# Kernel optimization log

Hardware: AMD Instinct MI355X
Metric: run time of the kernel (lower is better)

## Reference

```python
import jax, jax.numpy as jnp
import numpy as np

N_NODES = 10000
N_EDGES = 320000
D_IN = 256
D_OUT = 256


def setup_inputs() -> dict:
    key = jax.random.key(0)
    k1, k2, k3, k4, k5, k6 = jax.random.split(key, 6)
    feat = jax.random.normal(k1, (N_NODES, D_IN), dtype=jnp.float32)
    eweight = jax.random.uniform(k2, (N_EDGES, 1), dtype=jnp.float32)
    # Linear(in_dim*2 -> out_dim): weight [out, 2*in], bias [out]
    W = jax.random.normal(k3, (D_OUT, 2 * D_IN), dtype=jnp.float32) / np.sqrt(2 * D_IN)
    b = jax.random.normal(k4, (D_OUT,), dtype=jnp.float32) * 0.01
    src = jax.random.randint(k5, (N_EDGES,), 0, N_NODES, dtype=jnp.int64)
    dst = jax.random.randint(k6, (N_EDGES,), 0, N_NODES, dtype=jnp.int64)
    return {"feat": feat, "eweight": eweight, "W": W, "b": b, "src": src, "dst": dst}


def reference(feat, eweight, W, b, src, dst):
    n = feat.shape[0]
    # message: u_mul_e -> h[src] * ew   (broadcast [E,1] over [E,D])
    msg = feat[src] * eweight
    # mean reduce by destination: sum(msg) / in-degree
    agg = jax.ops.segment_sum(msg, dst, num_segments=n)
    deg = jax.ops.segment_sum(jnp.ones((src.shape[0],), dtype=feat.dtype), dst, num_segments=n)
    h_neigh = agg / jnp.maximum(deg, 1.0)[:, None]
    # concat aggregated with self features, then linear
    h = jnp.concatenate([h_neigh, feat], axis=-1)  # [N, 2*D]
    return h @ W.T + b
```

## Files before the change

### kernel.cpp

```cpp
#include <hip/hip_runtime.h>
#include <hip/hip_bf16.h>

#define N_NODES 10000
#define N_EDGES 320000
#define D 256
#define K_TOT 512
#define CAP 128

typedef __attribute__((ext_vector_type(8))) short bf16x8;
typedef __attribute__((ext_vector_type(4))) float f32x4;

__device__ __forceinline__ float bf2f(unsigned short u) {
  return __uint_as_float(((unsigned int)u) << 16);
}
__device__ __forceinline__ unsigned short f2bf(float f) {
  unsigned int x = __float_as_uint(f);
  unsigned int r = (x + 0x7fffu + ((x >> 16) & 1u)) >> 16;
  return (unsigned short)r;
}

#define FEAT_VECS (N_NODES * D / 8)
#define W_VECS    (D * K_TOT / 8)
#define CUR_VECS  (N_NODES / 4)
__global__ __launch_bounds__(256) void tobf16_kernel(
    const float* __restrict__ feat, const float* __restrict__ W,
    unsigned short* __restrict__ hcat, unsigned short* __restrict__ Wb,
    int* __restrict__ cursor) {
  int gid = blockIdx.x * 256 + threadIdx.x;
  const float* srcp;
  unsigned short* dstp;
  if (gid < FEAT_VECS) {
    int row = gid >> 5;
    int v = gid & 31;
    srcp = feat + (size_t)row * D + v * 8;
    dstp = hcat + (size_t)row * K_TOT + D + v * 8;
  } else if (gid < FEAT_VECS + W_VECS) {
    int g = gid - FEAT_VECS;
    int row = g >> 6;
    int v = g & 63;
    srcp = W + (size_t)row * K_TOT + v * 8;
    dstp = Wb + (size_t)row * K_TOT + v * 8;
  } else if (gid < FEAT_VECS + W_VECS + CUR_VECS) {
    int g = gid - (FEAT_VECS + W_VECS);
    reinterpret_cast<int4*>(cursor)[g] = make_int4(0, 0, 0, 0);
    return;
  } else {
    return;
  }
  float4 a = reinterpret_cast<const float4*>(srcp)[0];
  float4 b = reinterpret_cast<const float4*>(srcp)[1];
  reinterpret_cast<ushort4*>(dstp)[0] =
      make_ushort4(f2bf(a.x), f2bf(a.y), f2bf(a.z), f2bf(a.w));
  reinterpret_cast<ushort4*>(dstp)[1] =
      make_ushort4(f2bf(b.x), f2bf(b.y), f2bf(b.z), f2bf(b.w));
}

__global__ __launch_bounds__(256) void append_kernel(const int* __restrict__ src,
                                                     const int* __restrict__ dst,
                                                     const float* __restrict__ ew,
                                                     int* __restrict__ cursor,
                                                     int2* __restrict__ bucket) {
  int i = (blockIdx.x * 256 + threadIdx.x) * 2;
  if (i + 1 < N_EDGES) {
    int2 s2 = *reinterpret_cast<const int2*>(src + i);
    int2 d2 = *reinterpret_cast<const int2*>(dst + i);
    float2 w2 = *reinterpret_cast<const float2*>(ew + i);
    int pos0 = atomicAdd(&cursor[d2.x], 1);
    if (pos0 < CAP)
      bucket[(size_t)d2.x * CAP + pos0] = make_int2(s2.x, __float_as_int(w2.x));
    int pos1 = atomicAdd(&cursor[d2.y], 1);
    if (pos1 < CAP)
      bucket[(size_t)d2.y * CAP + pos1] = make_int2(s2.y, __float_as_int(w2.y));
  } else if (i < N_EDGES) {
    int d = dst[i];
    int pos = atomicAdd(&cursor[d], 1);
    if (pos < CAP)
      bucket[(size_t)d * CAP + pos] = make_int2(src[i], __float_as_int(ew[i]));
  }
}

__global__ __launch_bounds__(256) void agg_kernel(const int* __restrict__ cursor,
                                                  const int2* __restrict__ bucket,
                                                  unsigned short* __restrict__ hcat) {
  int bid = blockIdx.x;
  int half = (bid >= 2500) ? 1 : 0;
  int nb = bid - half * 2500;
  int wave = threadIdx.x >> 6;
  int lane = threadIdx.x & 63;
  int node = nb * 4 + wave;
  if (node >= N_NODES) return;
  int cnt = cursor[node];
  int end = min(cnt, CAP);
  const int2* bk = bucket + (size_t)node * CAP;
  const unsigned short* fb = hcat + D + half * 128 + (size_t)lane * 2;
  float a0 = 0.f, a1 = 0.f;
  int i = 0;

#define G2(p, va, vb)                                                          \
    va = *reinterpret_cast<const ushort2*>(fb + (size_t)(p).x * K_TOT);        \
    vb = *reinterpret_cast<const ushort2*>(fb + (size_t)(p).z * K_TOT);
#define A1(v, wgt)                                                             \
    a0 += bf2f((v).x) * (wgt); a1 += bf2f((v).y) * (wgt);
#define AP(p, va, vb)                                                          \
    { float wa_ = __int_as_float((p).y), wb_ = __int_as_float((p).w);          \
      A1(va, wa_) A1(vb, wb_) }

  for (; i + 16 <= end; i += 16) {
    int4 p0 = *reinterpret_cast<const int4*>(bk + i);
    int4 p1 = *reinterpret_cast<const int4*>(bk + i + 2);
    int4 p2 = *reinterpret_cast<const int4*>(bk + i + 4);
    int4 p3 = *reinterpret_cast<const int4*>(bk + i + 6);
    int4 p4 = *reinterpret_cast<const int4*>(bk + i + 8);
    int4 p5 = *reinterpret_cast<const int4*>(bk + i + 10);
    int4 p6 = *reinterpret_cast<const int4*>(bk + i + 12);
    int4 p7 = *reinterpret_cast<const int4*>(bk + i + 14);
    ushort2 v0, v1, v2, v3, v4, v5, v6, v7, v8, v9, va, vb, vc, vd, ve, vf;
    G2(p0, v0, v1) G2(p1, v2, v3) G2(p2, v4, v5) G2(p3, v6, v7)
    G2(p4, v8, v9) G2(p5, va, vb) G2(p6, vc, vd) G2(p7, ve, vf)
    AP(p0, v0, v1) AP(p1, v2, v3) AP(p2, v4, v5) AP(p3, v6, v7)
    AP(p4, v8, v9) AP(p5, va, vb) AP(p6, vc, vd) AP(p7, ve, vf)
  }
  for (; i + 8 <= end; i += 8) {
    int4 p0 = *reinterpret_cast<const int4*>(bk + i);
    int4 p1 = *reinterpret_cast<const int4*>(bk + i + 2);
    int4 p2 = *reinterpret_cast<const int4*>(bk + i + 4);
    int4 p3 = *reinterpret_cast<const int4*>(bk + i + 6);
    ushort2 v0, v1, v2, v3, v4, v5, v6, v7;
    G2(p0, v0, v1) G2(p1, v2, v3) G2(p2, v4, v5) G2(p3, v6, v7)
    AP(p0, v0, v1) AP(p1, v2, v3) AP(p2, v4, v5) AP(p3, v6, v7)
  }
  for (; i < end; ++i) {
    int2 sw = bk[i];
    ushort2 v = *reinterpret_cast<const ushort2*>(fb + (size_t)sw.x * K_TOT);
    float wgt = __int_as_float(sw.y);
    A1(v, wgt)
  }
#undef G2
#undef A1
#undef AP

  float inv = 1.0f / fmaxf((float)cnt, 1.0f);
  ushort2 o;
  o.x = f2bf(a0 * inv);
  o.y = f2bf(a1 * inv);
  *reinterpret_cast<ushort2*>(hcat + (size_t)node * K_TOT + half * 128 + lane * 2) = o;
}

#define GBM 64
#define GBN 64
#define GBK 64
#define LPAD 72
#define RTILES 157

__global__ __launch_bounds__(256) void gemm_kernel(
    const unsigned short* __restrict__ hcat, const unsigned short* __restrict__ Wb,
    const float* __restrict__ bias, float* __restrict__ out) {
  __shared__ unsigned short As[GBM][LPAD];
  __shared__ unsigned short Bs[GBN][LPAD];

  int bid = blockIdx.x;
  int r, c;
  if (bid < 608) {
    int g = bid >> 5;
    int w8 = bid & 31;
    r = g * 8 + (w8 & 7);
    c = w8 >> 3;
  } else {
    int w8 = bid - 608;
    r = 152 + w8 % 5;
    c = w8 / 5;
  }
  int row0 = r * GBM;
  int col0 = c * GBN;

  int t = threadIdx.x;
  int lane = t & 63;
  int w = t >> 6;
  int wr = w >> 1;
  int wc = w & 1;
  int lhi = lane >> 4;
  int llo = lane & 15;

  f32x4 acc[2][2];
  #pragma unroll
  for (int m = 0; m < 2; ++m)
    #pragma unroll
    for (int n = 0; n < 2; ++n) acc[m][n] = (f32x4){0.f, 0.f, 0.f, 0.f};

  for (int k0 = 0; k0 < K_TOT; k0 += GBK) {
    #pragma unroll
    for (int it = 0; it < 2; ++it) {
      int idx = t + it * 256;
      int rr = idx >> 3;
      int kv = (idx & 7) * 8;
      int row = row0 + rr;
      uint4 v = make_uint4(0, 0, 0, 0);
      if (row < N_NODES)
        v = *reinterpret_cast<const uint4*>(hcat + (size_t)row * K_TOT + k0 + kv);
      *reinterpret_cast<uint4*>(&As[rr][kv]) = v;
    }
    #pragma unroll
    for (int it = 0; it < 2; ++it) {
      int idx = t + it * 256;
      int cc = idx >> 3;
      int kv = (idx & 7) * 8;
      uint4 v = *reinterpret_cast<const uint4*>(Wb + (size_t)(col0 + cc) * K_TOT + k0 + kv);
      *reinterpret_cast<uint4*>(&Bs[cc][kv]) = v;
    }
    __syncthreads();

    #pragma unroll
    for (int ks = 0; ks < 2; ++ks) {
      int ak = ks * 32 + lhi * 8;
      bf16x8 a[2], b[2];
      #pragma unroll
      for (int m = 0; m < 2; ++m)
        a[m] = *reinterpret_cast<const bf16x8*>(&As[wr * 32 + m * 16 + llo][ak]);
      #pragma unroll
      for (int n = 0; n < 2; ++n)
        b[n] = *reinterpret_cast<const bf16x8*>(&Bs[wc * 32 + n * 16 + llo][ak]);
      #pragma unroll
      for (int m = 0; m < 2; ++m)
        #pragma unroll
        for (int n = 0; n < 2; ++n)
          acc[m][n] = __builtin_amdgcn_mfma_f32_16x16x32_bf16(a[m], b[n], acc[m][n], 0, 0, 0);
    }
    __syncthreads();
  }

  #pragma unroll
  for (int m = 0; m < 2; ++m) {
    #pragma unroll
    for (int n = 0; n < 2; ++n) {
      int col = col0 + wc * 32 + n * 16 + llo;
      float bv = bias[col];
      #pragma unroll
      for (int rr = 0; rr < 4; ++rr) {
        int orow = row0 + wr * 32 + m * 16 + lhi * 4 + rr;
        if (orow < N_NODES)
          out[(size_t)orow * D + col] = acc[m][n][rr] + bv;
      }
    }
  }
}

extern "C" void kernel_launch(void* const* d_in, const int* in_sizes, int n_in,
                              void* d_out, int out_size, void* d_ws, size_t ws_size,
                              hipStream_t stream) {
  const float* feat = (const float*)d_in[0];
  const float* ew   = (const float*)d_in[1];
  const float* W    = (const float*)d_in[2];
  const float* bias = (const float*)d_in[3];
  const int*   src  = (const int*)d_in[4];
  const int*   dst  = (const int*)d_in[5];
  float* out = (float*)d_out;

  char* ws = (char*)d_ws;
  unsigned short* hcat = (unsigned short*)ws;  ws += (size_t)N_NODES * K_TOT * sizeof(unsigned short);
  unsigned short* Wb   = (unsigned short*)ws;  ws += (size_t)D * K_TOT * sizeof(unsigned short);
  int* cursor   = (int*)ws;                    ws += N_NODES * sizeof(int);
  int2* bucket  = (int2*)ws;                   ws += (size_t)N_NODES * CAP * sizeof(int2);

  tobf16_kernel<<<(FEAT_VECS + W_VECS + CUR_VECS + 255) / 256, 256, 0, stream>>>(
      feat, W, hcat, Wb, cursor);
  append_kernel<<<(N_EDGES / 2 + 255) / 256, 256, 0, stream>>>(src, dst, ew, cursor, bucket);
  agg_kernel<<<5000, 256, 0, stream>>>(cursor, bucket, hcat);

  gemm_kernel<<<RTILES * 4, 256, 0, stream>>>(hcat, Wb, bias, out);
}
```

Baseline: 70.87 us.

## Slice bf16 features into column-sliced layout for cache-local gather aggregation

The conversion kernel now also writes a copy of bf16 features in a slice-major layout (8 slices of 32 columns), so each slice forms a compact table that is more likely to fit in cache. The aggregation kernel is split into 8 column slices per node group; in each wave, four groups of 16 lanes handle different edges in parallel and combine their partial sums with shuffles. This is meant to improve L2 locality of the random gathers and raise edge-level parallelism, at the cost of an extra feature copy write, more blocks, and re-reading the bucket lists once per slice.

Result: slower. 84.54 us (+19.3%).

```diff
diff --git a/kernel.cpp b/kernel.cpp
--- a/kernel.cpp
+++ b/kernel.cpp
@@ -6,6 +6,8 @@
 #define D 256
 #define K_TOT 512
 #define CAP 128
+#define NSLICE 8
+#define SCH 32
 
 typedef __attribute__((ext_vector_type(8))) short bf16x8;
 typedef __attribute__((ext_vector_type(4))) float f32x4;
@@ -24,35 +26,38 @@
 #define CUR_VECS  (N_NODES / 4)
 __global__ __launch_bounds__(256) void tobf16_kernel(
     const float* __restrict__ feat, const float* __restrict__ W,
-    unsigned short* __restrict__ hcat, unsigned short* __restrict__ Wb,
-    int* __restrict__ cursor) {
+    unsigned short* __restrict__ featb, unsigned short* __restrict__ hcat,
+    unsigned short* __restrict__ Wb, int* __restrict__ cursor) {
   int gid = blockIdx.x * 256 + threadIdx.x;
-  const float* srcp;
-  unsigned short* dstp;
   if (gid < FEAT_VECS) {
     int row = gid >> 5;
     int v = gid & 31;
-    srcp = feat + (size_t)row * D + v * 8;
-    dstp = hcat + (size_t)row * K_TOT + D + v * 8;
+    const float* srcp = feat + (size_t)row * D + v * 8;
+    float4 a = reinterpret_cast<const float4*>(srcp)[0];
+    float4 b = reinterpret_cast<const float4*>(srcp)[1];
+    ushort4 o0 = make_ushort4(f2bf(a.x), f2bf(a.y), f2bf(a.z), f2bf(a.w));
+    ushort4 o1 = make_ushort4(f2bf(b.x), f2bf(b.y), f2bf(b.z), f2bf(b.w));
+    unsigned short* dh = hcat + (size_t)row * K_TOT + D + v * 8;
+    reinterpret_cast<ushort4*>(dh)[0] = o0;
+    reinterpret_cast<ushort4*>(dh)[1] = o1;
+    int s = v >> 2;
+    unsigned short* ds = featb + ((size_t)s * N_NODES + row) * SCH + (v & 3) * 8;
+    reinterpret_cast<ushort4*>(ds)[0] = o0;
+    reinterpret_cast<ushort4*>(ds)[1] = o1;
   } else if (gid < FEAT_VECS + W_VECS) {
     int g = gid - FEAT_VECS;
-    int row = g >> 6;
-    int v = g & 63;
-    srcp = W + (size_t)row * K_TOT + v * 8;
-    dstp = Wb + (size_t)row * K_TOT + v * 8;
+    const float* srcp = W + (size_t)g * 8;
+    unsigned short* dstp = Wb + (size_t)g * 8;
+    float4 a = reinterpret_cast<const float4*>(srcp)[0];
+    float4 b = reinterpret_cast<const float4*>(srcp)[1];
+    reinterpret_cast<ushort4*>(dstp)[0] =
+        make_ushort4(f2bf(a.x), f2bf(a.y), f2bf(a.z), f2bf(a.w));
+    reinterpret_cast<ushort4*>(dstp)[1] =
+        make_ushort4(f2bf(b.x), f2bf(b.y), f2bf(b.z), f2bf(b.w));
   } else if (gid < FEAT_VECS + W_VECS + CUR_VECS) {
     int g = gid - (FEAT_VECS + W_VECS);
     reinterpret_cast<int4*>(cursor)[g] = make_int4(0, 0, 0, 0);
-    return;
-  } else {
-    return;
-  }
-  float4 a = reinterpret_cast<const float4*>(srcp)[0];
-  float4 b = reinterpret_cast<const float4*>(srcp)[1];
-  reinterpret_cast<ushort4*>(dstp)[0] =
-      make_ushort4(f2bf(a.x), f2bf(a.y), f2bf(a.z), f2bf(a.w));
-  reinterpret_cast<ushort4*>(dstp)[1] =
-      make_ushort4(f2bf(b.x), f2bf(b.y), f2bf(b.z), f2bf(b.w));
+  }
 }
 
 __global__ __launch_bounds__(256) void append_kernel(const int* __restrict__ src,
@@ -81,69 +86,53 @@
 
 __global__ __launch_bounds__(256) void agg_kernel(const int* __restrict__ cursor,
                                                   const int2* __restrict__ bucket,
+                                                  const unsigned short* __restrict__ featb,
                                                   unsigned short* __restrict__ hcat) {
-  int bid = blockIdx.x;
-  int half = (bid >= 2500) ? 1 : 0;
-  int nb = bid - half * 2500;
-  int wave = threadIdx.x >> 6;
+  int b = blockIdx.x;
+  int s = b & 7;
+  int g = b >> 3;
+  int wv = threadIdx.x >> 6;
   int lane = threadIdx.x & 63;
-  int node = nb * 4 + wave;
-  if (node >= N_NODES) return;
+  int node = g * 4 + wv;
+  int q = lane >> 4;
+  int c2 = lane & 15;
   int cnt = cursor[node];
   int end = min(cnt, CAP);
   const int2* bk = bucket + (size_t)node * CAP;
-  const unsigned short* fb = hcat + D + half * 128 + (size_t)lane * 2;
+  const unsigned short* fs = featb + (size_t)s * N_NODES * SCH + c2 * 2;
   float a0 = 0.f, a1 = 0.f;
-  int i = 0;
-
-#define G2(p, va, vb)                                                          \
-    va = *reinterpret_cast<const ushort2*>(fb + (size_t)(p).x * K_TOT);        \
-    vb = *reinterpret_cast<const ushort2*>(fb + (size_t)(p).z * K_TOT);
-#define A1(v, wgt)                                                             \
-    a0 += bf2f((v).x) * (wgt); a1 += bf2f((v).y) * (wgt);
-#define AP(p, va, vb)                                                          \
-    { float wa_ = __int_as_float((p).y), wb_ = __int_as_float((p).w);          \
-      A1(va, wa_) A1(vb, wb_) }
-
-  for (; i + 16 <= end; i += 16) {
-    int4 p0 = *reinterpret_cast<const int4*>(bk + i);
-    int4 p1 = *reinterpret_cast<const int4*>(bk + i + 2);
-    int4 p2 = *reinterpret_cast<const int4*>(bk + i + 4);
-    int4 p3 = *reinterpret_cast<const int4*>(bk + i + 6);
-    int4 p4 = *reinterpret_cast<const int4*>(bk + i + 8);
-    int4 p5 = *reinterpret_cast<const int4*>(bk + i + 10);
-    int4 p6 = *reinterpret_cast<const int4*>(bk + i + 12);
-    int4 p7 = *reinterpret_cast<const int4*>(bk + i + 14);
-    ushort2 v0, v1, v2, v3, v4, v5, v6, v7, v8, v9, va, vb, vc, vd, ve, vf;
-    G2(p0, v0, v1) G2(p1, v2, v3) G2(p2, v4, v5) G2(p3, v6, v7)
-    G2(p4, v8, v9) G2(p5, va, vb) G2(p6, vc, vd) G2(p7, ve, vf)
-    AP(p0, v0, v1) AP(p1, v2, v3) AP(p2, v4, v5) AP(p3, v6, v7)
-    AP(p4, v8, v9) AP(p5, va, vb) AP(p6, vc, vd) AP(p7, ve, vf)
-  }
-  for (; i + 8 <= end; i += 8) {
-    int4 p0 = *reinterpret_cast<const int4*>(bk + i);
-    int4 p1 = *reinterpret_cast<const int4*>(bk + i + 2);
-    int4 p2 = *reinterpret_cast<const int4*>(bk + i + 4);
-    int4 p3 = *reinterpret_cast<const int4*>(bk + i + 6);
-    ushort2 v0, v1, v2, v3, v4, v5, v6, v7;
-    G2(p0, v0, v1) G2(p1, v2, v3) G2(p2, v4, v5) G2(p3, v6, v7)
-    AP(p0, v0, v1) AP(p1, v2, v3) AP(p2, v4, v5) AP(p3, v6, v7)
-  }
-  for (; i < end; ++i) {
-    int2 sw = bk[i];
-    ushort2 v = *reinterpret_cast<const ushort2*>(fb + (size_t)sw.x * K_TOT);
-    float wgt = __int_as_float(sw.y);
-    A1(v, wgt)
-  }
-#undef G2
-#undef A1
-#undef AP
-
-  float inv = 1.0f / fmaxf((float)cnt, 1.0f);
-  ushort2 o;
-  o.x = f2bf(a0 * inv);
-  o.y = f2bf(a1 * inv);
-  *reinterpret_cast<ushort2*>(hcat + (size_t)node * K_TOT + half * 128 + lane * 2) = o;
+
+  for (int i = 0; i < end; i += 16) {
+    int i0 = i + q, i1 = i + 4 + q, i2 = i + 8 + q, i3 = i + 12 + q;
+    bool v0 = i0 < end, v1 = i1 < end, v2 = i2 < end, v3 = i3 < end;
+    int2 p0 = bk[v0 ? i0 : 0];
+    int2 p1 = bk[v1 ? i1 : 0];
+    int2 p2 = bk[v2 ? i2 : 0];
+    int2 p3 = bk[v3 ? i3 : 0];
+    ushort2 x0 = *reinterpret_cast<const ushort2*>(fs + (size_t)p0.x * SCH);
+    ushort2 x1 = *reinterpret_cast<const ushort2*>(fs + (size_t)p1.x * SCH);
+    ushort2 x2 = *reinterpret_cast<const ushort2*>(fs + (size_t)p2.x * SCH);
+    ushort2 x3 = *reinterpret_cast<const ushort2*>(fs + (size_t)p3.x * SCH);
+    float w0 = v0 ? __int_as_float(p0.y) : 0.f;
+    float w1 = v1 ? __int_as_float(p1.y) : 0.f;
+    float w2 = v2 ? __int_as_float(p2.y) : 0.f;
+    float w3 = v3 ? __int_as_float(p3.y) : 0.f;
+    a0 += bf2f(x0.x) * w0; a1 += bf2f(x0.y) * w0;
+    a0 += bf2f(x1.x) * w1; a1 += bf2f(x1.y) * w1;
+    a0 += bf2f(x2.x) * w2; a1 += bf2f(x2.y) * w2;
+    a0 += bf2f(x3.x) * w3; a1 += bf2f(x3.y) * w3;
+  }
+
+  a0 += __shfl_xor(a0, 16); a1 += __shfl_xor(a1, 16);
+  a0 += __shfl_xor(a0, 32); a1 += __shfl_xor(a1, 32);
+
+  if (lane < 16) {
+    float inv = 1.0f / fmaxf((float)cnt, 1.0f);
+    ushort2 o;
+    o.x = f2bf(a0 * inv);
+    o.y = f2bf(a1 * inv);
+    *reinterpret_cast<ushort2*>(hcat + (size_t)node * K_TOT + s * SCH + c2 * 2) = o;
+  }
 }
 
 #define GBM 64
@@ -256,15 +245,15 @@
   float* out = (float*)d_out;
 
   char* ws = (char*)d_ws;
-  unsigned short* hcat = (unsigned short*)ws;  ws += (size_t)N_NODES * K_TOT * sizeof(unsigned short);
-  unsigned short* Wb   = (unsigned short*)ws;  ws += (size_t)D * K_TOT * sizeof(unsigned short);
+  unsigned short* featb = (unsigned short*)ws; ws += (size_t)NSLICE * N_NODES * SCH * sizeof(unsigned short);
+  unsigned short* hcat  = (unsigned short*)ws; ws += (size_t)N_NODES * K_TOT * sizeof(unsigned short);
+  unsigned short* Wb    = (unsigned short*)ws; ws += (size_t)D * K_TOT * sizeof(unsigned short);
   int* cursor   = (int*)ws;                    ws += N_NODES * sizeof(int);
   int2* bucket  = (int2*)ws;                   ws += (size_t)N_NODES * CAP * sizeof(int2);
 
   tobf16_kernel<<<(FEAT_VECS + W_VECS + CUR_VECS + 255) / 256, 256, 0, stream>>>(
-      feat, W, hcat, Wb, cursor);
+      feat, W, featb, hcat, Wb, cursor);
   append_kernel<<<(N_EDGES / 2 + 255) / 256, 256, 0, stream>>>(src, dst, ew, cursor, bucket);
-  agg_kernel<<<5000, 256, 0, stream>>>(cursor, bucket, hcat);
-
+  agg_kernel<<<2500 * NSLICE, 256, 0, stream>>>(cursor, bucket, featb, hcat);
   gemm_kernel<<<RTILES * 4, 256, 0, stream>>>(hcat, Wb, bias, out);
 }
```
